# Optimization experiments

Measured on AMD Instinct MI355X. Metric: run time of the kernel, lower is better.

The kernel has to match this reference:

```python
import jax, jax.numpy as jnp
import numpy as np

B, S, D, H = 2, 2048, 1024, 16
d = D // H          # per-head dim (chunk along feature dim)
SEQ_LEN = 1024      # config.seq_len mask width
SCALE = float(np.sqrt(D))  # post-softmax divide by sqrt(model_dimension)
LN_EPS = 1e-5


def setup_inputs() -> dict:
    key = jax.random.key(0)
    ks = jax.random.split(key, 10)
    init = lambda k, shape: (jax.random.normal(k, shape, dtype=jnp.float32) * 0.02)
    return {
        "x": jax.random.normal(ks[0], (B, S, D), dtype=jnp.float32),
        "Wq": init(ks[1], (H, d, d)), "bq": jnp.zeros((H, d), jnp.float32),
        "Wk": init(ks[2], (H, d, d)), "bk": jnp.zeros((H, d), jnp.float32),
        "Wv": init(ks[3], (H, d, d)), "bv": jnp.zeros((H, d), jnp.float32),
        "Wo": init(ks[4], (D, D)),    "bo": jnp.zeros((D,), jnp.float32),
        "ln_g": jnp.ones((D,), jnp.float32),
        "ln_b": jnp.zeros((D,), jnp.float32),
    }


def reference(x, Wq, bq, Wk, bk, Wv, bv, Wo, bo, ln_g, ln_b):
    # chunk along feature dim == reshape D -> (H, d) since chunks are contiguous
    xh = x.reshape(B, S, H, d)                                  # [B,S,H,d]
    q = jnp.einsum('bshd,hde->bshe', xh, Wq) + bq               # [B,S,H,d]
    k = jnp.einsum('bshd,hde->bshe', xh, Wk) + bk
    v = jnp.einsum('bshd,hde->bshe', xh, Wv) + bv
    scores = jnp.einsum('bshd,bthd->bhst', q, k)                # [B,H,S,S]
    # custom mask: last query row, last SEQ_LEN key columns -> -inf
    scores = scores.at[:, :, -1, -SEQ_LEN:].set(-jnp.inf)
    attn = jax.nn.softmax(scores, axis=-1) / SCALE              # post-softmax scale
    o = jnp.einsum('bhst,bthd->bshd', attn, v).reshape(B, S, D) # concat heads
    proj = jnp.einsum('bsd,de->bse', o, Wo) + bo                # output projection
    y = x + proj                                                 # residual
    mu = jnp.mean(y, axis=-1, keepdims=True)
    var = jnp.mean(jnp.square(y - mu), axis=-1, keepdims=True)
    return (y - mu) * jax.lax.rsqrt(var + LN_EPS) * ln_g + ln_b
```

## Files before the change

### kernel.cpp

```cpp
#include <hip/hip_runtime.h>
#include <math.h>

#define B 2
#define S 2048
#define D 1024
#define H 16
#define HD 64
#define LN_EPS 1e-5f
#define LOG2E 1.44269504f
#define KSPLIT 2
#define NTS (S / 64 / KSPLIT)

typedef __bf16 bf16x8 __attribute__((ext_vector_type(8)));
typedef float f32x4 __attribute__((ext_vector_type(4)));

#if defined(__has_builtin)
#if __has_builtin(__builtin_amdgcn_exp2f)
#define EXP2(x) __builtin_amdgcn_exp2f(x)
#endif
#endif
#ifndef EXP2
#define EXP2(x) __expf((x) * 0.6931471805599453f)
#endif

__device__ __forceinline__ ushort f2bf(float f) {
    uint u = __float_as_uint(f);
    u += 0x7FFFu + ((u >> 16) & 1u);
    return (ushort)(u >> 16);
}

__device__ __forceinline__ bf16x8 ldfrag(const char* base, int row, int cbyte) {
    int a = row * 128 + (cbyte ^ ((row & 7) << 4));
    union { uint4 u; bf16x8 v; } c;
    c.u = *(const uint4*)(base + a);
    return c.v;
}

__global__ __launch_bounds__(256) void wo_cvt_kernel(
        const float* __restrict__ Wo, ushort* __restrict__ wt) {
    __shared__ float t[64][65];
    int tid = threadIdx.x;
    int r0 = blockIdx.y * 64, c0 = blockIdx.x * 64;
#pragma unroll
    for (int it = 0; it < 16; ++it) {
        int idx = tid + 256 * it;
        int row = idx >> 6, col = idx & 63;
        t[row][col] = Wo[(size_t)(r0 + row) * D + c0 + col];
    }
    __syncthreads();
#pragma unroll
    for (int it = 0; it < 16; ++it) {
        int idx = tid + 256 * it;
        int nrow = idx >> 6, kcol = idx & 63;
        wt[(size_t)(c0 + nrow) * D + r0 + kcol] = f2bf(t[kcol][nrow]);
    }
}

__global__ __launch_bounds__(256) void wqkv_cvt_kernel(
        const float* __restrict__ Wq, const float* __restrict__ Wk,
        const float* __restrict__ Wv,
        ushort* __restrict__ wqt, ushort* __restrict__ wkt, ushort* __restrict__ wvt) {
    __shared__ float t[64][65];
    int h = blockIdx.x, which = blockIdx.y;
    const float* W = (which == 0) ? Wq : (which == 1) ? Wk : Wv;
    ushort* out = (which == 0) ? wqt : (which == 1) ? wkt : wvt;
    int tid = threadIdx.x;
    const float* Wh = W + h * HD * HD;
    ushort* oh = out + h * HD * HD;
#pragma unroll
    for (int it = 0; it < 16; ++it) {
        int idx = tid + 256 * it;
        t[idx >> 6][idx & 63] = Wh[idx];
    }
    __syncthreads();
#pragma unroll
    for (int it = 0; it < 16; ++it) {
        int idx = tid + 256 * it;
        int e = idx >> 6, dd = idx & 63;
        oh[idx] = f2bf(t[dd][e]);
    }
}

__global__ __launch_bounds__(256) void qkv_kernel(
        const float* __restrict__ x,
        const ushort* __restrict__ wqt, const ushort* __restrict__ wkt,
        const ushort* __restrict__ wvt,
        const float* __restrict__ bq, const float* __restrict__ bk,
        const float* __restrict__ bv,
        ushort* __restrict__ qh, ushort* __restrict__ kh, ushort* __restrict__ vth) {
    __shared__ char xt[16384];
    const int tid = threadIdx.x;
    const int w = tid >> 6, l = tid & 63;
    const int lg = l >> 4, lr = l & 15;
    const int h = blockIdx.y;
    const size_t row0 = (size_t)blockIdx.x * 128;
    const int b = (int)(row0 >> 11);
    const int s0 = (int)(row0 & (S - 1));
    const size_t hb = (size_t)b * H + h;

#pragma unroll
    for (int it = 0; it < 4; ++it) {
        int c = tid + 256 * it;
        int row = c >> 3, sub = c & 7;
        const float* src = x + (row0 + row) * D + h * HD + 8 * sub;
        float4 f0 = *(const float4*)src;
        float4 f1 = *(const float4*)(src + 4);
        uint2 lo = make_uint2((uint)f2bf(f0.x) | ((uint)f2bf(f0.y) << 16),
                              (uint)f2bf(f0.z) | ((uint)f2bf(f0.w) << 16));
        uint2 hi = make_uint2((uint)f2bf(f1.x) | ((uint)f2bf(f1.y) << 16),
                              (uint)f2bf(f1.z) | ((uint)f2bf(f1.w) << 16));
        int p0 = 64 * (sub >> 2) + 32 * (sub & 1) + 8 * ((sub >> 1) & 1);
        int sz = (row & 7) << 4;
        char* dst = xt + row * 128;
        *(uint2*)(dst + (p0 ^ sz)) = lo;
        *(uint2*)(dst + ((p0 + 16) ^ sz)) = hi;
    }
    __syncthreads();

    bf16x8 xa[2][2];
#pragma unroll
    for (int fm = 0; fm < 2; ++fm)
#pragma unroll
        for (int ks = 0; ks < 2; ++ks)
            xa[fm][ks] = ldfrag(xt, 32 * w + 16 * fm + lr, 64 * ks + 16 * lg);

#pragma unroll
    for (int tsel = 0; tsel < 3; ++tsel) {
        const ushort* wsrc = (tsel == 0) ? wqt : (tsel == 1) ? wkt : wvt;
        const float* bsrc = (tsel == 0) ? bq : (tsel == 1) ? bk : bv;
        bf16x8 wf[4][2];
#pragma unroll
        for (int fn = 0; fn < 4; ++fn) {
            const char* wp = (const char*)(wsrc + ((size_t)h * HD + 16 * fn + lr) * HD);
#pragma unroll
            for (int ks = 0; ks < 2; ++ks) {
                uint2 a = *(const uint2*)(wp + 64 * ks + 8 * lg);
                uint2 c2 = *(const uint2*)(wp + 64 * ks + 8 * lg + 32);
                union { uint4 u; bf16x8 v; } cc;
                cc.u = make_uint4(a.x, a.y, c2.x, c2.y);
                wf[fn][ks] = cc.v;
            }
        }
        f32x4 acc[2][4];
#pragma unroll
        for (int fm = 0; fm < 2; ++fm)
#pragma unroll
            for (int fn = 0; fn < 4; ++fn)
#pragma unroll
                for (int r = 0; r < 4; ++r) acc[fm][fn][r] = 0.f;
#pragma unroll
        for (int fm = 0; fm < 2; ++fm)
#pragma unroll
            for (int fn = 0; fn < 4; ++fn)
#pragma unroll
                for (int ks = 0; ks < 2; ++ks)
                    acc[fm][fn] = __builtin_amdgcn_mfma_f32_16x16x32_bf16(
                        xa[fm][ks], wf[fn][ks], acc[fm][fn], 0, 0, 0);
        if (tsel == 0) {
#pragma unroll
            for (int fn = 0; fn < 4; ++fn) {
                float bias = bsrc[h * HD + 16 * fn + lr];
#pragma unroll
                for (int fm = 0; fm < 2; ++fm)
#pragma unroll
                    for (int r = 0; r < 4; ++r) {
                        int srow = s0 + 32 * w + 16 * fm + 4 * lg + r;
                        qh[(hb * S + srow) * HD + 16 * fn + lr] =
                            f2bf((acc[fm][fn][r] + bias) * LOG2E);
                    }
            }
        } else if (tsel == 1) {
#pragma unroll
            for (int fn = 0; fn < 4; ++fn) {
                float bias = bsrc[h * HD + 16 * fn + lr];
#pragma unroll
                for (int fm = 0; fm < 2; ++fm)
#pragma unroll
                    for (int r = 0; r < 4; ++r) {
                        int srow = s0 + 32 * w + 16 * fm + 4 * lg + r;
                        kh[(hb * S + srow) * HD + 16 * fn + lr] =
                            f2bf(acc[fm][fn][r] + bias);
                    }
            }
        } else {
#pragma unroll
            for (int fn = 0; fn < 4; ++fn) {
                float bias = bsrc[h * HD + 16 * fn + lr];
                int e = 16 * fn + lr;
#pragma unroll
                for (int fm = 0; fm < 2; ++fm) {
                    uint2 pk;
                    pk.x = (uint)f2bf(acc[fm][fn][0] + bias) |
                           ((uint)f2bf(acc[fm][fn][1] + bias) << 16);
                    pk.y = (uint)f2bf(acc[fm][fn][2] + bias) |
                           ((uint)f2bf(acc[fm][fn][3] + bias) << 16);
                    *(uint2*)(vth + (hb * HD + e) * S + s0 + 32 * w + 16 * fm + 4 * lg) = pk;
                }
            }
        }
    }
}

__global__ __launch_bounds__(512) void attn_kernel(
        const ushort* __restrict__ qh, const ushort* __restrict__ kh,
        const ushort* __restrict__ vth, ushort* __restrict__ ou,
        float* __restrict__ ls) {
    __shared__ char kt[3][8192];
    __shared__ char vt[3][8192];
    const int tid = threadIdx.x;
    const int w = tid >> 6, l = tid & 63;
    const int lg = l >> 4, lr = l & 15;
    const int ksp = blockIdx.y;
    const int h = blockIdx.z & (H - 1), b = blockIdx.z >> 4;
    const int q0 = blockIdx.x * 256 + 32 * w;
    const size_t bh = (size_t)b * H + h;
    const ushort* qbase = qh + bh * S * HD;
    const ushort* kbase = kh + bh * S * HD;
    const ushort* vbase = vth + bh * HD * S;

    const int r0s = tid >> 3, ssub = tid & 7;
    const int sp0 = 64 * (ssub >> 2) + 32 * (ssub & 1) + 8 * ((ssub >> 1) & 1);
    const int ssz = (r0s & 7) << 4;

    bf16x8 qf[2][2];
#pragma unroll
    for (int fn = 0; fn < 2; ++fn) {
        const char* qp = (const char*)(qbase + (size_t)(q0 + 16 * fn + lr) * HD);
#pragma unroll
        for (int ks = 0; ks < 2; ++ks) {
            uint2 xlo = *(const uint2*)(qp + 64 * ks + 8 * lg);
            uint2 xhi = *(const uint2*)(qp + 64 * ks + 8 * lg + 32);
            union { uint4 u; bf16x8 v; } c;
            c.u = make_uint4(xlo.x, xlo.y, xhi.x, xhi.y);
            qf[fn][ks] = c.v;
        }
    }

    f32x4 acc[2][4];
#pragma unroll
    for (int fn = 0; fn < 2; ++fn)
#pragma unroll
        for (int n0 = 0; n0 < 4; ++n0)
#pragma unroll
            for (int r = 0; r < 4; ++r) acc[fn][n0][r] = 0.f;
    f32x4 accs[2];
#pragma unroll
    for (int fn = 0; fn < 2; ++fn)
#pragma unroll
        for (int r = 0; r < 4; ++r) accs[fn][r] = 0.f;
    const f32x4 z4 = {0.f, 0.f, 0.f, 0.f};
    bf16x8 onef;
#pragma unroll
    for (int j = 0; j < 8; ++j) onef[j] = (__bf16)1.0f;
    const bool lastq = (q0 + 32 == S) && (lr == 15);

    {
        const int kv0 = ksp * NTS * 64;
        uint4 kd = *(const uint4*)(kbase + (size_t)(kv0 + r0s) * HD + 8 * ssub);
        uint4 vd = *(const uint4*)(vbase + (size_t)r0s * S + kv0 + 8 * ssub);
        char* kr = kt[0] + r0s * 128;
        char* vr = vt[0] + r0s * 128;
        *(uint2*)(kr + (sp0 ^ ssz)) = make_uint2(kd.x, kd.y);
        *(uint2*)(kr + ((sp0 + 16) ^ ssz)) = make_uint2(kd.z, kd.w);
        *(uint2*)(vr + (sp0 ^ ssz)) = make_uint2(vd.x, vd.y);
        *(uint2*)(vr + ((sp0 + 16) ^ ssz)) = make_uint2(vd.z, vd.w);
    }
    __syncthreads();

    int cur = 0;
    for (int t = 0; t < NTS; ++t) {
        const int kv0 = (ksp * NTS + t) * 64;
        int nxt = cur + 1; if (nxt == 3) nxt = 0;
        uint4 kd2, vd2;
        if (t + 1 < NTS) {
            kd2 = *(const uint4*)(kbase + (size_t)(kv0 + 64 + r0s) * HD + 8 * ssub);
            vd2 = *(const uint4*)(vbase + (size_t)r0s * S + kv0 + 64 + 8 * ssub);
        }

        const char* ktb = kt[cur];
        const char* vtb = vt[cur];
        __builtin_amdgcn_s_setprio(1);
        f32x4 s[4][2];
#pragma unroll
        for (int fm = 0; fm < 4; ++fm) {
            bf16x8 k0 = ldfrag(ktb, fm * 16 + lr, 16 * lg);
            bf16x8 k1 = ldfrag(ktb, fm * 16 + lr, 64 + 16 * lg);
#pragma unroll
            for (int fn = 0; fn < 2; ++fn) {
                s[fm][fn] = __builtin_amdgcn_mfma_f32_16x16x32_bf16(k0, qf[fn][0], z4, 0, 0, 0);
                s[fm][fn] = __builtin_amdgcn_mfma_f32_16x16x32_bf16(k1, qf[fn][1], s[fm][fn], 0, 0, 0);
            }
        }
        if (lastq && kv0 >= S - 1024) {
#pragma unroll
            for (int fm = 0; fm < 4; ++fm)
#pragma unroll
                for (int r = 0; r < 4; ++r) s[fm][1][r] = -INFINITY;
        }

        bf16x8 pa[2][2];
#pragma unroll
        for (int fn = 0; fn < 2; ++fn)
#pragma unroll
            for (int ks = 0; ks < 2; ++ks)
#pragma unroll
                for (int j = 0; j < 8; ++j)
                    pa[fn][ks][j] = (__bf16)EXP2(s[(j >> 2) + 2 * ks][fn][j & 3]);
#pragma unroll
        for (int fn = 0; fn < 2; ++fn) {
            accs[fn] = __builtin_amdgcn_mfma_f32_16x16x32_bf16(pa[fn][0], onef, accs[fn], 0, 0, 0);
            accs[fn] = __builtin_amdgcn_mfma_f32_16x16x32_bf16(pa[fn][1], onef, accs[fn], 0, 0, 0);
        }
#pragma unroll
        for (int n0 = 0; n0 < 4; ++n0) {
            bf16x8 v0 = ldfrag(vtb, n0 * 16 + lr, 16 * lg);
            bf16x8 v1 = ldfrag(vtb, n0 * 16 + lr, 64 + 16 * lg);
#pragma unroll
            for (int fn = 0; fn < 2; ++fn) {
                acc[fn][n0] = __builtin_amdgcn_mfma_f32_16x16x32_bf16(pa[fn][0], v0, acc[fn][n0], 0, 0, 0);
                acc[fn][n0] = __builtin_amdgcn_mfma_f32_16x16x32_bf16(pa[fn][1], v1, acc[fn][n0], 0, 0, 0);
            }
        }
        __builtin_amdgcn_s_setprio(0);

        if (t + 1 < NTS) {
            char* kr = kt[nxt] + r0s * 128;
            char* vr = vt[nxt] + r0s * 128;
            *(uint2*)(kr + (sp0 ^ ssz)) = make_uint2(kd2.x, kd2.y);
            *(uint2*)(kr + ((sp0 + 16) ^ ssz)) = make_uint2(kd2.z, kd2.w);
            *(uint2*)(vr + (sp0 ^ ssz)) = make_uint2(vd2.x, vd2.y);
            *(uint2*)(vr + ((sp0 + 16) ^ ssz)) = make_uint2(vd2.z, vd2.w);
            __syncthreads();
        }
        cur = nxt;
    }

#pragma unroll
    for (int fn = 0; fn < 2; ++fn)
#pragma unroll
        for (int r = 0; r < 4; ++r) {
            int qrow = q0 + 16 * fn + 4 * lg + r;
            ushort* op = ou + (((size_t)ksp * B + b) * S + qrow) * D + h * HD;
#pragma unroll
            for (int n0 = 0; n0 < 4; ++n0)
                op[n0 * 16 + lr] = f2bf(acc[fn][n0][r]);
            if (lr == 0)
                ls[(((size_t)ksp * B + b) * H + h) * S + qrow] = accs[fn][r];
        }
}

__global__ __launch_bounds__(256) void combine_kernel(
        const ushort* __restrict__ ou, const float* __restrict__ ls,
        ushort* __restrict__ ob) {
    int tid = threadIdx.x;
    size_t row = blockIdx.x;
    int b = (int)(row >> 11), s = (int)(row & (S - 1));
    int d0 = tid * 4, h = d0 >> 6;
    float lsum = 0.f;
#pragma unroll
    for (int ksp = 0; ksp < KSPLIT; ++ksp)
        lsum += ls[(((size_t)ksp * B + b) * H + h) * S + s];
    float inv = 1.0f / (lsum * 32.0f);
    float o0 = 0.f, o1 = 0.f, o2 = 0.f, o3 = 0.f;
#pragma unroll
    for (int ksp = 0; ksp < KSPLIT; ++ksp) {
        ushort4 u = *(const ushort4*)(ou + (((size_t)ksp * B + b) * S + s) * D + d0);
        o0 += __uint_as_float((uint)u.x << 16);
        o1 += __uint_as_float((uint)u.y << 16);
        o2 += __uint_as_float((uint)u.z << 16);
        o3 += __uint_as_float((uint)u.w << 16);
    }
    ushort4 r;
    r.x = f2bf(o0 * inv); r.y = f2bf(o1 * inv);
    r.z = f2bf(o2 * inv); r.w = f2bf(o3 * inv);
    *(ushort4*)(ob + row * D + d0) = r;
}

__global__ __launch_bounds__(256) void proj_gemm_kernel(
        const ushort* __restrict__ ob, const ushort* __restrict__ wt,
        const float* __restrict__ x, const float* __restrict__ bo,
        float* __restrict__ yws) {
    __shared__ char at[3][16384];
    __shared__ char btl[3][8192];
    const int tid = threadIdx.x;
    const int w = tid >> 6, l = tid & 63;
    const int lg = l >> 4, lr = l & 15;
    const int wr = w >> 1, wc = w & 1;
    const int m0 = blockIdx.y * 128;
    const int n0 = blockIdx.x * 64;

    const ushort* srcp[6];
    int off1[6], off2[6], whichB[6];
#pragma unroll
    for (int it = 0; it < 6; ++it) {
        int c = tid + 256 * it;
        int row, sub;
        if (c < 1024) {
            row = c >> 3; sub = c & 7;
            srcp[it] = ob + (size_t)(m0 + row) * D + 8 * sub;
            whichB[it] = 0;
        } else {
            int c2 = c - 1024;
            row = c2 >> 3; sub = c2 & 7;
            srcp[it] = wt + (size_t)(n0 + row) * D + 8 * sub;
            whichB[it] = 1;
        }
        int p0 = 64 * (sub >> 2) + 32 * (sub & 1) + 8 * ((sub >> 1) & 1);
        int sz = (row & 7) << 4;
        off1[it] = row * 128 + (p0 ^ sz);
        off2[it] = row * 128 + ((p0 + 16) ^ sz);
    }

    f32x4 acc[4][2];
#pragma unroll
    for (int fm = 0; fm < 4; ++fm)
#pragma unroll
        for (int fn = 0; fn < 2; ++fn)
#pragma unroll
            for (int r = 0; r < 4; ++r) acc[fm][fn][r] = 0.f;

    uint4 pf[6];
#pragma unroll
    for (int it = 0; it < 6; ++it) pf[it] = *(const uint4*)(srcp[it]);
#pragma unroll
    for (int it = 0; it < 6; ++it) {
        char* base = whichB[it] ? btl[0] : at[0];
        *(uint2*)(base + off1[it]) = make_uint2(pf[it].x, pf[it].y);
        *(uint2*)(base + off2[it]) = make_uint2(pf[it].z, pf[it].w);
    }
    __syncthreads();

    int cur = 0;
    for (int t = 0; t < D / 64; ++t) {
        int nxt = cur + 1; if (nxt == 3) nxt = 0;
        if (t + 1 < D / 64) {
#pragma unroll
            for (int it = 0; it < 6; ++it)
                pf[it] = *(const uint4*)(srcp[it] + (size_t)(t + 1) * 64);
        }

        bf16x8 af[4][2], bfr[2][2];
#pragma unroll
        for (int fm = 0; fm < 4; ++fm)
#pragma unroll
            for (int ks = 0; ks < 2; ++ks)
                af[fm][ks] = ldfrag(at[cur], 64 * wr + 16 * fm + lr, 64 * ks + 16 * lg);
#pragma unroll
        for (int fn = 0; fn < 2; ++fn)
#pragma unroll
            for (int ks = 0; ks < 2; ++ks)
                bfr[fn][ks] = ldfrag(btl[cur], 32 * wc + 16 * fn + lr, 64 * ks + 16 * lg);
#pragma unroll
        for (int fm = 0; fm < 4; ++fm)
#pragma unroll
            for (int fn = 0; fn < 2; ++fn)
#pragma unroll
                for (int ks = 0; ks < 2; ++ks)
                    acc[fm][fn] = __builtin_amdgcn_mfma_f32_16x16x32_bf16(
                        af[fm][ks], bfr[fn][ks], acc[fm][fn], 0, 0, 0);

        if (t + 1 < D / 64) {
#pragma unroll
            for (int it = 0; it < 6; ++it) {
                char* base = whichB[it] ? btl[nxt] : at[nxt];
                *(uint2*)(base + off1[it]) = make_uint2(pf[it].x, pf[it].y);
                *(uint2*)(base + off2[it]) = make_uint2(pf[it].z, pf[it].w);
            }
            __syncthreads();
        }
        cur = nxt;
    }

#pragma unroll
    for (int fm = 0; fm < 4; ++fm)
#pragma unroll
        for (int fn = 0; fn < 2; ++fn) {
            int col = n0 + 32 * wc + 16 * fn + lr;
            float bov = bo[col];
#pragma unroll
            for (int r = 0; r < 4; ++r) {
                int rowg = m0 + 64 * wr + 16 * fm + 4 * lg + r;
                size_t off = (size_t)rowg * D + col;
                yws[off] = acc[fm][fn][r] + x[off] + bov;
            }
        }
}

__global__ __launch_bounds__(256) void ln_kernel(
        const float* __restrict__ yws, const float* __restrict__ g,
        const float* __restrict__ bb, float* __restrict__ out) {
    __shared__ float rs[4], rq[4];
    int tid = threadIdx.x;
    size_t row = blockIdx.x;
    float4 yv = *(const float4*)(yws + row * D + tid * 4);
    float s = yv.x + yv.y + yv.z + yv.w;
    float q = yv.x * yv.x + yv.y * yv.y + yv.z * yv.z + yv.w * yv.w;
    for (int off = 32; off > 0; off >>= 1) {
        s += __shfl_down(s, off, 64);
        q += __shfl_down(q, off, 64);
    }
    if ((tid & 63) == 0) { rs[tid >> 6] = s; rq[tid >> 6] = q; }
    __syncthreads();
    float sum = rs[0] + rs[1] + rs[2] + rs[3];
    float sq  = rq[0] + rq[1] + rq[2] + rq[3];
    float mean = sum * (1.0f / D);
    float var  = sq * (1.0f / D) - mean * mean;
    float rstd = rsqrtf(var + LN_EPS);
    float4 gv = *(const float4*)(g + tid * 4);
    float4 bv = *(const float4*)(bb + tid * 4);
    float4 ov;
    ov.x = (yv.x - mean) * rstd * gv.x + bv.x;
    ov.y = (yv.y - mean) * rstd * gv.y + bv.y;
    ov.z = (yv.z - mean) * rstd * gv.z + bv.z;
    ov.w = (yv.w - mean) * rstd * gv.w + bv.w;
    *(float4*)(out + row * D + tid * 4) = ov;
}

extern "C" void kernel_launch(void* const* d_in, const int* in_sizes, int n_in,
                              void* d_out, int out_size, void* d_ws, size_t ws_size,
                              hipStream_t stream) {
    const float* x  = (const float*)d_in[0];
    const float* Wq = (const float*)d_in[1];
    const float* bq = (const float*)d_in[2];
    const float* Wk = (const float*)d_in[3];
    const float* bk = (const float*)d_in[4];
    const float* Wv = (const float*)d_in[5];
    const float* bv = (const float*)d_in[6];
    const float* Wo = (const float*)d_in[7];
    const float* bo = (const float*)d_in[8];
    const float* g  = (const float*)d_in[9];
    const float* bb = (const float*)d_in[10];
    float* out = (float*)d_out;

    const size_t NBD = (size_t)B * S * D;
    ushort* qh  = (ushort*)d_ws;
    ushort* kh  = qh + NBD;
    ushort* vth = kh + NBD;
    ushort* ob  = vth + NBD;
    ushort* wt  = ob + NBD;
    ushort* wqt = wt + (size_t)D * D;
    ushort* wkt = wqt + H * HD * HD;
    ushort* wvt = wkt + H * HD * HD;
    ushort* ou  = wvt + H * HD * HD;
    float*  ls  = (float*)(ou + (size_t)KSPLIT * NBD);
    float*  yws = (float*)d_ws;

    wo_cvt_kernel<<<dim3(16, 16), 256, 0, stream>>>(Wo, wt);
    wqkv_cvt_kernel<<<dim3(H, 3), 256, 0, stream>>>(Wq, Wk, Wv, wqt, wkt, wvt);
    qkv_kernel<<<dim3((B * S) / 128, H), 256, 0, stream>>>(
        x, wqt, wkt, wvt, bq, bk, bv, qh, kh, vth);
    attn_kernel<<<dim3(S / 256, KSPLIT, H * B), 512, 0, stream>>>(qh, kh, vth, ou, ls);
    combine_kernel<<<dim3(B * S), 256, 0, stream>>>(ou, ls, ob);
    proj_gemm_kernel<<<dim3(D / 64, (B * S) / 128), 256, 0, stream>>>(ob, wt, x, bo, yws);
    ln_kernel<<<dim3(B * S), 256, 0, stream>>>(yws, g, bb, out);
}
```

Measured before the change: 98.34 us.

## Fuse split-K combine into projection GEMM loads and merge weight conversion kernels

The separate combine kernel, which merged the two split-K attention partials and wrote a bf16 buffer, is removed. The projection GEMM now loads both partials and the row sums directly, then normalizes and converts them while staging the A tile. The GEMM tile shape changes from 128x64 to 64x128, and the two weight-conversion kernels are merged into one launch. This saves a full intermediate write and read plus two launches, but the GEMM reads twice the A data per tile and does the combine arithmetic redundantly across N-blocks.

```diff
diff --git a/kernel.cpp b/kernel.cpp
--- a/kernel.cpp
+++ b/kernel.cpp
@@ -10,6 +10,8 @@
 #define LOG2E 1.44269504f
 #define KSPLIT 2
 #define NTS (S / 64 / KSPLIT)
+#define NBD_ELEMS (B * S * D)
+#define BHS_ELEMS (B * H * S)
 
 typedef __bf16 bf16x8 __attribute__((ext_vector_type(8)));
 typedef float f32x4 __attribute__((ext_vector_type(4)));
@@ -36,48 +38,53 @@
     return c.v;
 }
 
-__global__ __launch_bounds__(256) void wo_cvt_kernel(
-        const float* __restrict__ Wo, ushort* __restrict__ wt) {
+__device__ __forceinline__ uint comb2(uint a, uint b, float inv) {
+    float lo = (__uint_as_float(a << 16) + __uint_as_float(b << 16)) * inv;
+    float hi = (__uint_as_float(a & 0xFFFF0000u) + __uint_as_float(b & 0xFFFF0000u)) * inv;
+    return (uint)f2bf(lo) | ((uint)f2bf(hi) << 16);
+}
+
+__global__ __launch_bounds__(256) void cvt_kernel(
+        const float* __restrict__ Wo,
+        const float* __restrict__ Wq, const float* __restrict__ Wk,
+        const float* __restrict__ Wv,
+        ushort* __restrict__ wt, ushort* __restrict__ wqt,
+        ushort* __restrict__ wkt, ushort* __restrict__ wvt) {
     __shared__ float t[64][65];
     int tid = threadIdx.x;
-    int r0 = blockIdx.y * 64, c0 = blockIdx.x * 64;
-#pragma unroll
-    for (int it = 0; it < 16; ++it) {
-        int idx = tid + 256 * it;
-        int row = idx >> 6, col = idx & 63;
-        t[row][col] = Wo[(size_t)(r0 + row) * D + c0 + col];
-    }
-    __syncthreads();
-#pragma unroll
-    for (int it = 0; it < 16; ++it) {
-        int idx = tid + 256 * it;
-        int nrow = idx >> 6, kcol = idx & 63;
-        wt[(size_t)(c0 + nrow) * D + r0 + kcol] = f2bf(t[kcol][nrow]);
-    }
-}
-
-__global__ __launch_bounds__(256) void wqkv_cvt_kernel(
-        const float* __restrict__ Wq, const float* __restrict__ Wk,
-        const float* __restrict__ Wv,
-        ushort* __restrict__ wqt, ushort* __restrict__ wkt, ushort* __restrict__ wvt) {
-    __shared__ float t[64][65];
-    int h = blockIdx.x, which = blockIdx.y;
-    const float* W = (which == 0) ? Wq : (which == 1) ? Wk : Wv;
-    ushort* out = (which == 0) ? wqt : (which == 1) ? wkt : wvt;
-    int tid = threadIdx.x;
-    const float* Wh = W + h * HD * HD;
-    ushort* oh = out + h * HD * HD;
-#pragma unroll
-    for (int it = 0; it < 16; ++it) {
-        int idx = tid + 256 * it;
-        t[idx >> 6][idx & 63] = Wh[idx];
-    }
-    __syncthreads();
-#pragma unroll
-    for (int it = 0; it < 16; ++it) {
-        int idx = tid + 256 * it;
-        int e = idx >> 6, dd = idx & 63;
-        oh[idx] = f2bf(t[dd][e]);
+    if (blockIdx.y < 16) {
+        int r0 = blockIdx.y * 64, c0 = blockIdx.x * 64;
+#pragma unroll
+        for (int it = 0; it < 16; ++it) {
+            int idx = tid + 256 * it;
+            int row = idx >> 6, col = idx & 63;
+            t[row][col] = Wo[(size_t)(r0 + row) * D + c0 + col];
+        }
+        __syncthreads();
+#pragma unroll
+        for (int it = 0; it < 16; ++it) {
+            int idx = tid + 256 * it;
+            int nrow = idx >> 6, kcol = idx & 63;
+            wt[(size_t)(c0 + nrow) * D + r0 + kcol] = f2bf(t[kcol][nrow]);
+        }
+    } else {
+        int h = blockIdx.x, which = blockIdx.y - 16;
+        const float* W = (which == 0) ? Wq : (which == 1) ? Wk : Wv;
+        ushort* outp = (which == 0) ? wqt : (which == 1) ? wkt : wvt;
+        const float* Wh = W + h * HD * HD;
+        ushort* oh = outp + h * HD * HD;
+#pragma unroll
+        for (int it = 0; it < 16; ++it) {
+            int idx = tid + 256 * it;
+            t[idx >> 6][idx & 63] = Wh[idx];
+        }
+        __syncthreads();
+#pragma unroll
+        for (int it = 0; it < 16; ++it) {
+            int idx = tid + 256 * it;
+            int e = idx >> 6, dd = idx & 63;
+            oh[idx] = f2bf(t[dd][e]);
+        }
     }
 }
 
@@ -349,137 +356,135 @@
         }
 }
 
-__global__ __launch_bounds__(256) void combine_kernel(
+__global__ __launch_bounds__(256) void proj_gemm_kernel(
         const ushort* __restrict__ ou, const float* __restrict__ ls,
-        ushort* __restrict__ ob) {
-    int tid = threadIdx.x;
-    size_t row = blockIdx.x;
-    int b = (int)(row >> 11), s = (int)(row & (S - 1));
-    int d0 = tid * 4, h = d0 >> 6;
-    float lsum = 0.f;
-#pragma unroll
-    for (int ksp = 0; ksp < KSPLIT; ++ksp)
-        lsum += ls[(((size_t)ksp * B + b) * H + h) * S + s];
-    float inv = 1.0f / (lsum * 32.0f);
-    float o0 = 0.f, o1 = 0.f, o2 = 0.f, o3 = 0.f;
-#pragma unroll
-    for (int ksp = 0; ksp < KSPLIT; ++ksp) {
-        ushort4 u = *(const ushort4*)(ou + (((size_t)ksp * B + b) * S + s) * D + d0);
-        o0 += __uint_as_float((uint)u.x << 16);
-        o1 += __uint_as_float((uint)u.y << 16);
-        o2 += __uint_as_float((uint)u.z << 16);
-        o3 += __uint_as_float((uint)u.w << 16);
-    }
-    ushort4 r;
-    r.x = f2bf(o0 * inv); r.y = f2bf(o1 * inv);
-    r.z = f2bf(o2 * inv); r.w = f2bf(o3 * inv);
-    *(ushort4*)(ob + row * D + d0) = r;
-}
-
-__global__ __launch_bounds__(256) void proj_gemm_kernel(
-        const ushort* __restrict__ ob, const ushort* __restrict__ wt,
+        const ushort* __restrict__ wt,
         const float* __restrict__ x, const float* __restrict__ bo,
         float* __restrict__ yws) {
-    __shared__ char at[3][16384];
-    __shared__ char btl[3][8192];
+    __shared__ char at[3][8192];
+    __shared__ char btl[3][16384];
     const int tid = threadIdx.x;
     const int w = tid >> 6, l = tid & 63;
     const int lg = l >> 4, lr = l & 15;
     const int wr = w >> 1, wc = w & 1;
-    const int m0 = blockIdx.y * 128;
-    const int n0 = blockIdx.x * 64;
-
-    const ushort* srcp[6];
-    int off1[6], off2[6], whichB[6];
-#pragma unroll
-    for (int it = 0; it < 6; ++it) {
+    const int m0 = blockIdx.y * 64;
+    const int n0 = blockIdx.x * 128;
+
+    const ushort* srcA[2];
+    const float* lsp[2];
+    int offA1[2], offA2[2];
+#pragma unroll
+    for (int it = 0; it < 2; ++it) {
         int c = tid + 256 * it;
-        int row, sub;
-        if (c < 1024) {
-            row = c >> 3; sub = c & 7;
-            srcp[it] = ob + (size_t)(m0 + row) * D + 8 * sub;
-            whichB[it] = 0;
-        } else {
-            int c2 = c - 1024;
-            row = c2 >> 3; sub = c2 & 7;
-            srcp[it] = wt + (size_t)(n0 + row) * D + 8 * sub;
-            whichB[it] = 1;
-        }
+        int row = c >> 3, sub = c & 7;
+        int r = m0 + row;
+        srcA[it] = ou + (size_t)r * D + 8 * sub;
+        int b = r >> 11, s = r & (S - 1);
+        lsp[it] = ls + (size_t)b * H * S + s;
         int p0 = 64 * (sub >> 2) + 32 * (sub & 1) + 8 * ((sub >> 1) & 1);
         int sz = (row & 7) << 4;
-        off1[it] = row * 128 + (p0 ^ sz);
-        off2[it] = row * 128 + ((p0 + 16) ^ sz);
-    }
-
-    f32x4 acc[4][2];
-#pragma unroll
-    for (int fm = 0; fm < 4; ++fm)
-#pragma unroll
-        for (int fn = 0; fn < 2; ++fn)
+        offA1[it] = row * 128 + (p0 ^ sz);
+        offA2[it] = row * 128 + ((p0 + 16) ^ sz);
+    }
+    const ushort* srcB[4];
+    int offB1[4], offB2[4];
+#pragma unroll
+    for (int it = 0; it < 4; ++it) {
+        int c = tid + 256 * it;
+        int row = c >> 3, sub = c & 7;
+        srcB[it] = wt + (size_t)(n0 + row) * D + 8 * sub;
+        int p0 = 64 * (sub >> 2) + 32 * (sub & 1) + 8 * ((sub >> 1) & 1);
+        int sz = (row & 7) << 4;
+        offB1[it] = row * 128 + (p0 ^ sz);
+        offB2[it] = row * 128 + ((p0 + 16) ^ sz);
+    }
+
+    f32x4 acc[2][4];
+#pragma unroll
+    for (int fm = 0; fm < 2; ++fm)
+#pragma unroll
+        for (int fn = 0; fn < 4; ++fn)
 #pragma unroll
             for (int r = 0; r < 4; ++r) acc[fm][fn][r] = 0.f;
 
-    uint4 pf[6];
-#pragma unroll
-    for (int it = 0; it < 6; ++it) pf[it] = *(const uint4*)(srcp[it]);
-#pragma unroll
-    for (int it = 0; it < 6; ++it) {
-        char* base = whichB[it] ? btl[0] : at[0];
-        *(uint2*)(base + off1[it]) = make_uint2(pf[it].x, pf[it].y);
-        *(uint2*)(base + off2[it]) = make_uint2(pf[it].z, pf[it].w);
-    }
+    uint4 pa0[2], pa1[2], pb[4];
+    float pl0[2], pl1[2];
+
+    auto LOADT = [&](int t) {
+#pragma unroll
+        for (int it = 0; it < 2; ++it) {
+            pa0[it] = *(const uint4*)(srcA[it] + (size_t)t * 64);
+            pa1[it] = *(const uint4*)(srcA[it] + (size_t)NBD_ELEMS + (size_t)t * 64);
+            pl0[it] = lsp[it][(size_t)t * S];
+            pl1[it] = lsp[it][(size_t)BHS_ELEMS + (size_t)t * S];
+        }
+#pragma unroll
+        for (int it = 0; it < 4; ++it)
+            pb[it] = *(const uint4*)(srcB[it] + (size_t)t * 64);
+    };
+    auto STORET = [&](int buf) {
+#pragma unroll
+        for (int it = 0; it < 2; ++it) {
+            float inv = 1.0f / ((pl0[it] + pl1[it]) * 32.0f);
+            uint cx = comb2(pa0[it].x, pa1[it].x, inv);
+            uint cy = comb2(pa0[it].y, pa1[it].y, inv);
+            uint cz = comb2(pa0[it].z, pa1[it].z, inv);
+            uint cw = comb2(pa0[it].w, pa1[it].w, inv);
+            *(uint2*)(at[buf] + offA1[it]) = make_uint2(cx, cy);
+            *(uint2*)(at[buf] + offA2[it]) = make_uint2(cz, cw);
+        }
+#pragma unroll
+        for (int it = 0; it < 4; ++it) {
+            *(uint2*)(btl[buf] + offB1[it]) = make_uint2(pb[it].x, pb[it].y);
+            *(uint2*)(btl[buf] + offB2[it]) = make_uint2(pb[it].z, pb[it].w);
+        }
+    };
+
+    LOADT(0);
+    STORET(0);
     __syncthreads();
 
     int cur = 0;
     for (int t = 0; t < D / 64; ++t) {
         int nxt = cur + 1; if (nxt == 3) nxt = 0;
-        if (t + 1 < D / 64) {
-#pragma unroll
-            for (int it = 0; it < 6; ++it)
-                pf[it] = *(const uint4*)(srcp[it] + (size_t)(t + 1) * 64);
-        }
-
-        bf16x8 af[4][2], bfr[2][2];
-#pragma unroll
-        for (int fm = 0; fm < 4; ++fm)
+        if (t + 1 < D / 64) LOADT(t + 1);
+
+        bf16x8 af[2][2], bfr[4][2];
+#pragma unroll
+        for (int fm = 0; fm < 2; ++fm)
 #pragma unroll
             for (int ks = 0; ks < 2; ++ks)
-                af[fm][ks] = ldfrag(at[cur], 64 * wr + 16 * fm + lr, 64 * ks + 16 * lg);
-#pragma unroll
-        for (int fn = 0; fn < 2; ++fn)
+                af[fm][ks] = ldfrag(at[cur], 32 * wr + 16 * fm + lr, 64 * ks + 16 * lg);
+#pragma unroll
+        for (int fn = 0; fn < 4; ++fn)
 #pragma unroll
             for (int ks = 0; ks < 2; ++ks)
-                bfr[fn][ks] = ldfrag(btl[cur], 32 * wc + 16 * fn + lr, 64 * ks + 16 * lg);
-#pragma unroll
-        for (int fm = 0; fm < 4; ++fm)
-#pragma unroll
-            for (int fn = 0; fn < 2; ++fn)
+                bfr[fn][ks] = ldfrag(btl[cur], 64 * wc + 16 * fn + lr, 64 * ks + 16 * lg);
+#pragma unroll
+        for (int fm = 0; fm < 2; ++fm)
+#pragma unroll
+            for (int fn = 0; fn < 4; ++fn)
 #pragma unroll
                 for (int ks = 0; ks < 2; ++ks)
                     acc[fm][fn] = __builtin_amdgcn_mfma_f32_16x16x32_bf16(
                         af[fm][ks], bfr[fn][ks], acc[fm][fn], 0, 0, 0);
 
         if (t + 1 < D / 64) {
-#pragma unroll
-            for (int it = 0; it < 6; ++it) {
-                char* base = whichB[it] ? btl[nxt] : at[nxt];
-                *(uint2*)(base + off1[it]) = make_uint2(pf[it].x, pf[it].y);
-                *(uint2*)(base + off2[it]) = make_uint2(pf[it].z, pf[it].w);
-            }
+            STORET(nxt);
             __syncthreads();
         }
         cur = nxt;
     }
 
 #pragma unroll
-    for (int fm = 0; fm < 4; ++fm)
-#pragma unroll
-        for (int fn = 0; fn < 2; ++fn) {
-            int col = n0 + 32 * wc + 16 * fn + lr;
+    for (int fm = 0; fm < 2; ++fm)
+#pragma unroll
+        for (int fn = 0; fn < 4; ++fn) {
+            int col = n0 + 64 * wc + 16 * fn + lr;
             float bov = bo[col];
 #pragma unroll
             for (int r = 0; r < 4; ++r) {
-                int rowg = m0 + 64 * wr + 16 * fm + 4 * lg + r;
+                int rowg = m0 + 32 * wr + 16 * fm + 4 * lg + r;
                 size_t off = (size_t)rowg * D + col;
                 yws[off] = acc[fm][fn][r] + x[off] + bov;
             }
@@ -536,8 +541,7 @@
     ushort* qh  = (ushort*)d_ws;
     ushort* kh  = qh + NBD;
     ushort* vth = kh + NBD;
-    ushort* ob  = vth + NBD;
-    ushort* wt  = ob + NBD;
+    ushort* wt  = vth + NBD;
     ushort* wqt = wt + (size_t)D * D;
     ushort* wkt = wqt + H * HD * HD;
     ushort* wvt = wkt + H * HD * HD;
@@ -545,12 +549,10 @@
     float*  ls  = (float*)(ou + (size_t)KSPLIT * NBD);
     float*  yws = (float*)d_ws;
 
-    wo_cvt_kernel<<<dim3(16, 16), 256, 0, stream>>>(Wo, wt);
-    wqkv_cvt_kernel<<<dim3(H, 3), 256, 0, stream>>>(Wq, Wk, Wv, wqt, wkt, wvt);
+    cvt_kernel<<<dim3(16, 19), 256, 0, stream>>>(Wo, Wq, Wk, Wv, wt, wqt, wkt, wvt);
     qkv_kernel<<<dim3((B * S) / 128, H), 256, 0, stream>>>(
         x, wqt, wkt, wvt, bq, bk, bv, qh, kh, vth);
     attn_kernel<<<dim3(S / 256, KSPLIT, H * B), 512, 0, stream>>>(qh, kh, vth, ou, ls);
-    combine_kernel<<<dim3(B * S), 256, 0, stream>>>(ou, ls, ob);
-    proj_gemm_kernel<<<dim3(D / 64, (B * S) / 128), 256, 0, stream>>>(ob, wt, x, bo, yws);
+    proj_gemm_kernel<<<dim3(D / 128, (B * S) / 64), 256, 0, stream>>>(ou, ls, wt, x, bo, yws);
     ln_kernel<<<dim3(B * S), 256, 0, stream>>>(yws, g, bb, out);
 }
```

Result: no change. 98.22 us (-0.1%).
